# Kernel optimization log

Hardware: AMD Instinct MI355X
Metric: run time of the kernel (lower is better)

Reference implementation:

```python
import jax, jax.numpy as jnp
import numpy as np

N = 100000
E = 1600000
IN_C = 128
HID = 32
HEADS = 4
OUT_C = 16
G = 128
NEG_SLOPE = 0.2


def setup_inputs() -> dict:
    key = jax.random.key(0)
    ks = jax.random.split(key, 16)
    x = jax.random.normal(ks[0], (N, IN_C), dtype=jnp.float32)
    edge_index = jax.random.randint(ks[1], (2, E), 0, N, dtype=jnp.int64)
    batch = jnp.sort(jax.random.randint(ks[2], (N,), 0, G, dtype=jnp.int64))
    node_weights = jax.random.uniform(ks[3], (N, 1), dtype=jnp.float32)
    s = 1.0 / np.sqrt(IN_C)
    W1 = jax.random.uniform(ks[4], (IN_C, HEADS * HID), jnp.float32, -s, s)
    att_src1 = jax.random.uniform(ks[5], (HEADS, HID), jnp.float32, -s, s)
    att_dst1 = jax.random.uniform(ks[6], (HEADS, HID), jnp.float32, -s, s)
    b1 = jnp.zeros((HEADS * HID,), jnp.float32)
    s2 = 1.0 / np.sqrt(HEADS * HID)
    W2 = jax.random.uniform(ks[7], (HEADS * HID, HID), jnp.float32, -s2, s2)
    att_src2 = jax.random.uniform(ks[8], (1, HID), jnp.float32, -s2, s2)
    att_dst2 = jax.random.uniform(ks[9], (1, HID), jnp.float32, -s2, s2)
    b2 = jnp.zeros((HID,), jnp.float32)
    s3 = 1.0 / np.sqrt(HID)
    fcW = jax.random.uniform(ks[10], (HID, OUT_C), jnp.float32, -s3, s3)
    fcb = jax.random.uniform(ks[11], (OUT_C,), jnp.float32, -s3, s3)
    return {"x": x, "edge_index": edge_index, "batch": batch,
            "node_weights": node_weights,
            "W1": W1, "att_src1": att_src1, "att_dst1": att_dst1, "b1": b1,
            "W2": W2, "att_src2": att_src2, "att_dst2": att_dst2, "b2": b2,
            "fcW": fcW, "fcb": fcb}


def gat_conv(x, src, dst, W, att_src, att_dst, bias, heads, ch, concat):
    n = x.shape[0]
    h = (x @ W).reshape(n, heads, ch)                       # [N,H,C]
    a_src = jnp.sum(h * att_src[None], axis=-1)             # [N,H]
    a_dst = jnp.sum(h * att_dst[None], axis=-1)             # [N,H]
    e = jax.nn.leaky_relu(a_src[src] + a_dst[dst], NEG_SLOPE)  # [E,H]
    # segment softmax over incoming edges of each destination node
    e_max = jax.ops.segment_max(e, dst, num_segments=n)
    ex = jnp.exp(e - e_max[dst])
    denom = jax.ops.segment_sum(ex, dst, num_segments=n)
    alpha = ex / denom[dst]                                 # [E,H]
    msg = h[src] * alpha[..., None]                         # [E,H,C]
    out = jax.ops.segment_sum(msg, dst, num_segments=n)     # [N,H,C]
    if concat:
        out = out.reshape(n, heads * ch)
    else:
        out = out.mean(axis=1)
    return out + bias


def reference(x, edge_index, batch, node_weights,
              W1, att_src1, att_dst1, b1,
              W2, att_src2, att_dst2, b2,
              fcW, fcb):
    n = x.shape[0]
    # PyG GATConv adds self-loops by default
    loop = jnp.arange(n, dtype=edge_index.dtype)
    src = jnp.concatenate([edge_index[0], loop])
    dst = jnp.concatenate([edge_index[1], loop])

    h = x * node_weights
    h = jax.nn.elu(gat_conv(h, src, dst, W1, att_src1, att_dst1, b1, HEADS, HID, True))
    h = jax.nn.elu(gat_conv(h, src, dst, W2, att_src2, att_dst2, b2, 1, HID, False))
    # global mean pool over graphs
    sums = jax.ops.segment_sum(h, batch, num_segments=G)
    cnts = jax.ops.segment_sum(jnp.ones((n,), h.dtype), batch, num_segments=G)
    pooled = sums / jnp.maximum(cnts, 1.0)[:, None]
    return pooled @ fcW + fcb
```

## Files before the change

### kernel.cpp

```cpp
#include <hip/hip_runtime.h>
#include <cstdint>

#define OUT_C 16
#define NGRAPH 128
#define NEG 0.2f
#define NB_MAX 512
#define BSH 8
#define BSZ 256
#define CAP 8192

typedef unsigned int uint;
typedef unsigned short ushort;
typedef unsigned char uchar;
typedef __attribute__((ext_vector_type(8))) short bf16x8;
typedef __attribute__((ext_vector_type(4))) float f32x4;
typedef __attribute__((ext_vector_type(2))) float f32x2;

union U4B { uint4 u; bf16x8 v; };

__device__ __forceinline__ ushort f2bf(float f) {
  uint u = __float_as_uint(f);
  uint r = (u + 0x7FFF + ((u >> 16) & 1)) >> 16;
  return (ushort)r;
}

__device__ __forceinline__ int wave_incl_scan_i(int v) {
  int lane = threadIdx.x & 63;
#pragma unroll
  for (int off = 1; off < 64; off <<= 1) {
    int u = __shfl_up(v, off, 64);
    if (lane >= off) v += u;
  }
  return v;
}

__global__ void k_bin(const int* __restrict__ ei,
                      const float* __restrict__ W1, const float* __restrict__ W2,
                      ushort* __restrict__ Wt1, ushort* __restrict__ Wt2,
                      int E, int Etot, int NB, int nbin,
                      int* __restrict__ bcur, uint* __restrict__ bbuf) {
  if (blockIdx.x >= nbin) {
    int t2 = (blockIdx.x - nbin) * 256 + threadIdx.x;
    if (t2 < 16384) {
      int n = t2 >> 7, k = t2 & 127;
      Wt1[t2] = f2bf(W1[k * 128 + n]);
    } else {
      int u = t2 - 16384;
      int n = u >> 7, k = u & 127;
      Wt2[u] = f2bf(W2[k * 32 + n]);
    }
    return;
  }
  __shared__ int h[NB_MAX];
  __shared__ int baseo[NB_MAX];
  int t = threadIdx.x;
  for (int b = t; b < NB; b += 256) h[b] = 0;
  __syncthreads();
  int cbase = blockIdx.x * 4096;
  int cend = min(cbase + 4096, Etot);
  for (int e = cbase + t; e < cend; e += 256) {
    int d = (e < E) ? ei[E + e] : (e - E);
    atomicAdd(&h[d >> BSH], 1);
  }
  __syncthreads();
  for (int b = t; b < NB; b += 256) {
    int c = h[b];
    baseo[b] = c ? atomicAdd(&bcur[b], c) : 0;
    h[b] = 0;
  }
  __syncthreads();
  for (int e = cbase + t; e < cend; e += 256) {
    int s, d;
    if (e < E) { s = ei[e]; d = ei[E + e]; } else { s = e - E; d = s; }
    int b = d >> BSH;
    int r = atomicAdd(&h[b], 1);
    bbuf[(size_t)b * CAP + baseo[b] + r] = ((uint)(d & (BSZ - 1)) << 17) | (uint)s;
  }
}

__global__ void k_build(const uint* __restrict__ bbuf, const int* __restrict__ bcur,
                        int NB, int N, int* __restrict__ offs, int* __restrict__ ssrc) {
  __shared__ int sst[NB_MAX + 1];
  __shared__ int wsum2[4];
  __shared__ int deg[BSZ];
  int t = threadIdx.x, lane = t & 63, wid = t >> 6;
  int v0 = (2 * t < NB) ? bcur[2 * t] : 0;
  int v1 = (2 * t + 1 < NB) ? bcur[2 * t + 1] : 0;
  int s = v0 + v1;
  int sv = wave_incl_scan_i(s);
  if (lane == 63) wsum2[wid] = sv;
  deg[t] = 0;
  __syncthreads();
  if (t == 0) {
    int r = 0;
#pragma unroll
    for (int k = 0; k < 4; k++) { int x = wsum2[k]; wsum2[k] = r; r += x; }
  }
  __syncthreads();
  int excl = wsum2[wid] + sv - s;
  sst[2 * t] = excl;
  sst[2 * t + 1] = excl + v0;
  if (t == 255) sst[512] = excl + v0 + v1;
  __syncthreads();
  int b = blockIdx.x;
  int ebeg = sst[b], eend = sst[b + 1];
  int cnt = eend - ebeg;
  for (int i = t; i < cnt; i += BSZ)
    atomicAdd(&deg[bbuf[(size_t)b * CAP + i] >> 17], 1);
  __syncthreads();
  int v = deg[t];
  int sv2 = wave_incl_scan_i(v);
  if (lane == 63) wsum2[wid] = sv2;
  __syncthreads();
  if (t == 0) {
    int r = 0;
#pragma unroll
    for (int k = 0; k < 4; k++) { int x = wsum2[k]; wsum2[k] = r; r += x; }
  }
  __syncthreads();
  int excl2 = wsum2[wid] + sv2 - v;
  int node = (b << BSH) + t;
  if (node < N) offs[node] = ebeg + excl2;
  if (b == 0 && t == 0) offs[N] = sst[512];
  __syncthreads();
  deg[t] = excl2;
  __syncthreads();
  for (int i = t; i < cnt; i += BSZ) {
    uint rec = bbuf[(size_t)b * CAP + i];
    int r = atomicAdd(&deg[rec >> 17], 1);
    ssrc[ebeg + r] = (int)(rec & 0x1FFFF);
  }
}

__global__ void k_gemm1(const float* __restrict__ x, const ushort* __restrict__ Wt,
                        const float* __restrict__ nw, const float* __restrict__ att_s,
                        const float* __restrict__ att_d, uchar* __restrict__ hb1,
                        float* __restrict__ asrc, float* __restrict__ adst, int M) {
  int wv = threadIdx.x >> 6, l = threadIdx.x & 63;
  int lg = l >> 4, lr = l & 15;
  int row0 = blockIdx.x * 64 + wv * 16;
  int node = row0 + lr;
  bool valid = node < M;
  float sc = valid ? nw[node] : 0.f;
  bf16x8 afr[4];
  const float* xr = x + (size_t)node * 128;
#pragma unroll
  for (int kc = 0; kc < 4; kc++) {
    float v[8];
    if (valid) {
      float4 q0 = *reinterpret_cast<const float4*>(xr + kc * 32 + lg * 8);
      float4 q1 = *reinterpret_cast<const float4*>(xr + kc * 32 + lg * 8 + 4);
      v[0] = q0.x; v[1] = q0.y; v[2] = q0.z; v[3] = q0.w;
      v[4] = q1.x; v[5] = q1.y; v[6] = q1.z; v[7] = q1.w;
    } else {
#pragma unroll
      for (int j = 0; j < 8; j++) v[j] = 0.f;
    }
    U4B a;
    uint pk0 = (uint)f2bf(v[0] * sc) | ((uint)f2bf(v[1] * sc) << 16);
    uint pk1 = (uint)f2bf(v[2] * sc) | ((uint)f2bf(v[3] * sc) << 16);
    uint pk2 = (uint)f2bf(v[4] * sc) | ((uint)f2bf(v[5] * sc) << 16);
    uint pk3 = (uint)f2bf(v[6] * sc) | ((uint)f2bf(v[7] * sc) << 16);
    a.u = make_uint4(pk0, pk1, pk2, pk3);
    afr[kc] = a.v;
  }
  float pS[4][4], pD[4][4];
#pragma unroll
  for (int h = 0; h < 4; h++)
#pragma unroll
    for (int v = 0; v < 4; v++) { pS[h][v] = 0.f; pD[h][v] = 0.f; }
#pragma unroll
  for (int ct = 0; ct < 8; ct++) {
    f32x4 acc = {0.f, 0.f, 0.f, 0.f};
    const ushort* wrow = Wt + (size_t)(ct * 16 + lr) * 128;
#pragma unroll
    for (int kc = 0; kc < 4; kc++) {
      U4B bfr;
      bfr.u = *reinterpret_cast<const uint4*>(wrow + kc * 32 + lg * 8);
      acc = __builtin_amdgcn_mfma_f32_16x16x32_bf16(afr[kc], bfr.v, acc, 0, 0, 0);
    }
    int col = ct * 16 + lr;
    float asw = att_s[col], adw = att_d[col];
    int h = ct >> 1;
#pragma unroll
    for (int v = 0; v < 4; v++) {
      int nrow = row0 + lg * 4 + v;
      if (nrow < M) {
        uint b8 = (uint)__builtin_amdgcn_cvt_pk_fp8_f32(acc[v], acc[v], 0, false);
        hb1[(size_t)nrow * 128 + col] = (uchar)(b8 & 0xFF);
      }
      pS[h][v] += acc[v] * asw;
      pD[h][v] += acc[v] * adw;
    }
  }
#pragma unroll
  for (int off = 1; off < 16; off <<= 1) {
#pragma unroll
    for (int h = 0; h < 4; h++)
#pragma unroll
      for (int v = 0; v < 4; v++) {
        pS[h][v] += __shfl_xor(pS[h][v], off, 16);
        pD[h][v] += __shfl_xor(pD[h][v], off, 16);
      }
  }
  if (lr == 0) {
#pragma unroll
    for (int v = 0; v < 4; v++) {
      int n2 = row0 + lg * 4 + v;
      if (n2 < M) {
#pragma unroll
        for (int h = 0; h < 4; h++) {
          asrc[n2 * 4 + h] = pS[h][v];
          adst[n2 * 4 + h] = pD[h][v];
        }
      }
    }
  }
}

__global__ void k_gemm2(const ushort* __restrict__ A, const ushort* __restrict__ Wt,
                        const float* __restrict__ att_s, const float* __restrict__ att_d,
                        uchar* __restrict__ hb2, float* __restrict__ asrc,
                        float* __restrict__ adst, int M) {
  int wv = threadIdx.x >> 6, l = threadIdx.x & 63;
  int lg = l >> 4, lr = l & 15;
  int row0 = blockIdx.x * 64 + wv * 16;
  int node = row0 + lr;
  bool valid = node < M;
  bf16x8 afr[4];
#pragma unroll
  for (int kc = 0; kc < 4; kc++) {
    U4B a;
    if (valid) a.u = *reinterpret_cast<const uint4*>(A + (size_t)node * 128 + kc * 32 + lg * 8);
    else a.u = make_uint4(0, 0, 0, 0);
    afr[kc] = a.v;
  }
  float pS[4], pD[4];
#pragma unroll
  for (int v = 0; v < 4; v++) { pS[v] = 0.f; pD[v] = 0.f; }
#pragma unroll
  for (int ct = 0; ct < 2; ct++) {
    f32x4 acc = {0.f, 0.f, 0.f, 0.f};
    const ushort* wrow = Wt + (size_t)(ct * 16 + lr) * 128;
#pragma unroll
    for (int kc = 0; kc < 4; kc++) {
      U4B bfr;
      bfr.u = *reinterpret_cast<const uint4*>(wrow + kc * 32 + lg * 8);
      acc = __builtin_amdgcn_mfma_f32_16x16x32_bf16(afr[kc], bfr.v, acc, 0, 0, 0);
    }
    int col = ct * 16 + lr;
    float asw = att_s[col], adw = att_d[col];
#pragma unroll
    for (int v = 0; v < 4; v++) {
      int nrow = row0 + lg * 4 + v;
      if (nrow < M) {
        uint b8 = (uint)__builtin_amdgcn_cvt_pk_fp8_f32(acc[v], acc[v], 0, false);
        hb2[(size_t)nrow * 32 + col] = (uchar)(b8 & 0xFF);
      }
      pS[v] += acc[v] * asw;
      pD[v] += acc[v] * adw;
    }
  }
#pragma unroll
  for (int off = 1; off < 16; off <<= 1) {
#pragma unroll
    for (int v = 0; v < 4; v++) {
      pS[v] += __shfl_xor(pS[v], off, 16);
      pD[v] += __shfl_xor(pD[v], off, 16);
    }
  }
  if (lr == 0) {
#pragma unroll
    for (int v = 0; v < 4; v++) {
      int n2 = row0 + lg * 4 + v;
      if (n2 < M) { asrc[n2] = pS[v]; adst[n2] = pD[v]; }
    }
  }
}

__global__ void k_aggr1(const int* __restrict__ offs, const int* __restrict__ ssrc,
                        const uchar* __restrict__ hb, const float* __restrict__ asrc,
                        const float* __restrict__ adst, const float* __restrict__ bias,
                        ushort* __restrict__ outb, int N) {
  int wid = threadIdx.x >> 6, l = threadIdx.x & 63;
  int d = blockIdx.x * 4 + wid;
  if (d >= N) return;
  int slot = l >> 3;
  int k = l & 7;
  int h = k >> 1;
  float ad = adst[d * 4 + h];
  int beg = offs[d], end = offs[d + 1];
  float a[16] = {};
  float ds = 0.f;
  for (int i = beg; i < end; i += 8) {
    int e = i + slot;
    int ec = min(e, end - 1);
    int s = ssrc[ec];
    float xv = asrc[s * 4 + h] + ad;
    xv = xv > 0.f ? xv : NEG * xv;
    float w = __expf(xv);
    w = (e < end) ? w : 0.f;
    uint4 p = *reinterpret_cast<const uint4*>(hb + (size_t)s * 128 + k * 16);
    uint pu[4] = {p.x, p.y, p.z, p.w};
#pragma unroll
    for (int q = 0; q < 4; q++) {
      f32x2 f0 = __builtin_amdgcn_cvt_pk_f32_fp8(pu[q], false);
      f32x2 f1 = __builtin_amdgcn_cvt_pk_f32_fp8(pu[q], true);
      a[q * 4 + 0] += w * f0.x;
      a[q * 4 + 1] += w * f0.y;
      a[q * 4 + 2] += w * f1.x;
      a[q * 4 + 3] += w * f1.y;
    }
    ds += w;
  }
  int b3 = (l >> 3) & 1, b4 = (l >> 4) & 1, b5 = (l >> 5) & 1;
  float t8[8];
#pragma unroll
  for (int r = 0; r < 8; r++) {
    float send = b3 ? a[r] : a[r + 8];
    float recv = __shfl_xor(send, 8, 64);
    t8[r] = (b3 ? a[r + 8] : a[r]) + recv;
  }
  float t4[4];
#pragma unroll
  for (int r = 0; r < 4; r++) {
    float send = b4 ? t8[r] : t8[r + 4];
    float recv = __shfl_xor(send, 16, 64);
    t4[r] = (b4 ? t8[r + 4] : t8[r]) + recv;
  }
  float t2[2];
#pragma unroll
  for (int r = 0; r < 2; r++) {
    float send = b5 ? t4[r] : t4[r + 2];
    float recv = __shfl_xor(send, 32, 64);
    t2[r] = (b5 ? t4[r + 2] : t4[r]) + recv;
  }
  ds += __shfl_xor(ds, 8, 64);
  ds += __shfl_xor(ds, 16, 64);
  ds += __shfl_xor(ds, 32, 64);
  float inv = 1.f / ds;
  int c0 = k * 16 + b3 * 8 + b4 * 4 + b5 * 2;
  float r0 = t2[0] * inv + bias[c0];
  float r1 = t2[1] * inv + bias[c0 + 1];
  r0 = r0 > 0.f ? r0 : expm1f(r0);
  r1 = r1 > 0.f ? r1 : expm1f(r1);
  *reinterpret_cast<uint*>(outb + (size_t)d * 128 + c0) =
      (uint)f2bf(r0) | ((uint)f2bf(r1) << 16);
}

__global__ void k_aggr2(const int* __restrict__ offs, const int* __restrict__ ssrc,
                        const uchar* __restrict__ hb, const float* __restrict__ asrc,
                        const float* __restrict__ adst, const float* __restrict__ bias,
                        float* __restrict__ out, int N) {
  int wid = threadIdx.x >> 6, l = threadIdx.x & 63;
  int d = blockIdx.x * 4 + wid;
  if (d >= N) return;
  int slot = l >> 2;
  int k = l & 3;
  float ad = adst[d];
  int beg = offs[d], end = offs[d + 1];
  float a[8] = {};
  float ds = 0.f;
  for (int i = beg; i < end; i += 16) {
    int e = i + slot;
    int ec = min(e, end - 1);
    int s = ssrc[ec];
    float xv = asrc[s] + ad;
    xv = xv > 0.f ? xv : NEG * xv;
    float w = __expf(xv);
    w = (e < end) ? w : 0.f;
    uint2 p = *reinterpret_cast<const uint2*>(hb + (size_t)s * 32 + k * 8);
    f32x2 f0 = __builtin_amdgcn_cvt_pk_f32_fp8(p.x, false);
    f32x2 f1 = __builtin_amdgcn_cvt_pk_f32_fp8(p.x, true);
    f32x2 f2 = __builtin_amdgcn_cvt_pk_f32_fp8(p.y, false);
    f32x2 f3 = __builtin_amdgcn_cvt_pk_f32_fp8(p.y, true);
    a[0] += w * f0.x; a[1] += w * f0.y; a[2] += w * f1.x; a[3] += w * f1.y;
    a[4] += w * f2.x; a[5] += w * f2.y; a[6] += w * f3.x; a[7] += w * f3.y;
    ds += w;
  }
  int b2 = (l >> 2) & 1, b3 = (l >> 3) & 1, b4 = (l >> 4) & 1;
  float t4[4];
#pragma unroll
  for (int r = 0; r < 4; r++) {
    float send = b2 ? a[r] : a[r + 4];
    float recv = __shfl_xor(send, 4, 64);
    t4[r] = (b2 ? a[r + 4] : a[r]) + recv;
  }
  float t2[2];
#pragma unroll
  for (int r = 0; r < 2; r++) {
    float send = b3 ? t4[r] : t4[r + 2];
    float recv = __shfl_xor(send, 8, 64);
    t2[r] = (b3 ? t4[r + 2] : t4[r]) + recv;
  }
  float send = b4 ? t2[0] : t2[1];
  float recv = __shfl_xor(send, 16, 64);
  float t1 = (b4 ? t2[1] : t2[0]) + recv;
  t1 += __shfl_xor(t1, 32, 64);
  ds += __shfl_xor(ds, 4, 64);
  ds += __shfl_xor(ds, 8, 64);
  ds += __shfl_xor(ds, 16, 64);
  ds += __shfl_xor(ds, 32, 64);
  if (l < 32) {
    int c = k * 8 + b2 * 4 + b3 * 2 + b4;
    float r = t1 / ds + bias[c];
    r = r > 0.f ? r : expm1f(r);
    out[(size_t)d * 32 + c] = r;
  }
}

__global__ void k_pool_fc(const float* __restrict__ h2, const int* __restrict__ batch,
                          const float* __restrict__ fcW, const float* __restrict__ fcb,
                          float* __restrict__ out, int N) {
  int g = blockIdx.x;
  int lo = 0, hi = N;
  while (lo < hi) { int mid = (lo + hi) >> 1; if (batch[mid] < g) lo = mid + 1; else hi = mid; }
  int beg = lo;
  hi = N;
  while (lo < hi) { int mid = (lo + hi) >> 1; if (batch[mid] < g + 1) lo = mid + 1; else hi = mid; }
  int end = lo;
  int t = threadIdx.x, c = t & 31, sub = t >> 5;
  float acc = 0.f;
  for (int n = beg + sub; n < end; n += 8) acc += h2[(size_t)n * 32 + c];
  __shared__ float red[8][32];
  __shared__ float pooled[32];
  red[sub][c] = acc;
  __syncthreads();
  if (sub == 0) {
    float s = 0.f;
#pragma unroll
    for (int i = 0; i < 8; i++) s += red[i][c];
    float cnt = (float)(end - beg);
    pooled[c] = s / fmaxf(cnt, 1.f);
  }
  __syncthreads();
  if (t < 16) {
    float r = fcb[t];
#pragma unroll
    for (int cc = 0; cc < 32; cc++) r += pooled[cc] * fcW[cc * 16 + t];
    out[g * 16 + t] = r;
  }
}

extern "C" void kernel_launch(void* const* d_in, const int* in_sizes, int n_in,
                              void* d_out, int out_size, void* d_ws, size_t ws_size,
                              hipStream_t stream) {
  const float* x     = (const float*)d_in[0];
  const int*   ei    = (const int*)d_in[1];
  const int*   batch = (const int*)d_in[2];
  const float* nw    = (const float*)d_in[3];
  const float* W1    = (const float*)d_in[4];
  const float* as1w  = (const float*)d_in[5];
  const float* ad1w  = (const float*)d_in[6];
  const float* b1    = (const float*)d_in[7];
  const float* W2    = (const float*)d_in[8];
  const float* as2w  = (const float*)d_in[9];
  const float* ad2w  = (const float*)d_in[10];
  const float* b2    = (const float*)d_in[11];
  const float* fcW   = (const float*)d_in[12];
  const float* fcb   = (const float*)d_in[13];
  float* out = (float*)d_out;

  const int N = in_sizes[0] / 128;
  const int E = in_sizes[1] / 2;
  const int Etot = E + N;
  const int NB = (N + BSZ - 1) >> BSH;

  char* w = (char*)d_ws;
  size_t ofs = 0;
  auto alloc = [&](size_t bytes) {
    char* p = w + ofs;
    ofs += (bytes + 255) & ~(size_t)255;
    return p;
  };
  uchar*  hb1    = (uchar*)alloc((size_t)N * 128);
  ushort* out1b  = (ushort*)alloc((size_t)N * 128 * 2);
  uchar*  hb2    = (uchar*)alloc((size_t)N * 32);
  float*  h2     = (float*)alloc((size_t)N * 32 * 4);
  float*  asrc1  = (float*)alloc((size_t)N * 4 * 4);
  float*  adst1  = (float*)alloc((size_t)N * 4 * 4);
  float*  asrc2  = (float*)alloc((size_t)N * 4);
  float*  adst2  = (float*)alloc((size_t)N * 4);
  ushort* Wt1    = (ushort*)alloc(16384 * 2);
  ushort* Wt2    = (ushort*)alloc(4096 * 2);
  int*    bcur   = (int*)alloc((size_t)NB * 4);
  int*    offs   = (int*)alloc((size_t)(N + 1) * 4);
  uint*   bbuf   = (uint*)alloc((size_t)NB * CAP * 4);
  int*    ssrc   = (int*)alloc((size_t)Etot * 4);

  hipMemsetAsync(bcur, 0, (size_t)NB * 4, stream);

  const int nbin = (Etot + 4095) / 4096;
  k_bin<<<nbin + 80, 256, 0, stream>>>(ei, W1, W2, Wt1, Wt2, E, Etot, NB, nbin, bcur, bbuf);
  k_build<<<NB, BSZ, 0, stream>>>(bbuf, bcur, NB, N, offs, ssrc);

  k_gemm1<<<(N + 63) / 64, 256, 0, stream>>>(x, Wt1, nw, as1w, ad1w, hb1, asrc1, adst1, N);
  k_aggr1<<<(N + 3) / 4, 256, 0, stream>>>(offs, ssrc, hb1, asrc1, adst1, b1, out1b, N);

  k_gemm2<<<(N + 63) / 64, 256, 0, stream>>>(out1b, Wt2, as2w, ad2w, hb2, asrc2, adst2, N);
  k_aggr2<<<(N + 3) / 4, 256, 0, stream>>>(offs, ssrc, hb2, asrc2, adst2, b2, h2, N);

  k_pool_fc<<<NGRAPH, 256, 0, stream>>>(h2, batch, fcW, fcb, out, N);
}
```

Baseline: 325.9 us.

## Merge CSR build with first GEMM and transpose MFMA output for packed stores

Fuses the CSR build kernel and the first-layer GEMM into one launch, with block ranges split by blockIdx, so the two independent stages can run concurrently on the GPU. Both GEMMs swap the MFMA operand order so each lane holds four consecutive columns of one node. That lets the fp8 output be written as one packed 32-bit store instead of four byte stores, and shortens the attention-score reduction to cross-lane-group shuffles with vectorized stores. This adds register pressure and a larger fused kernel, and concurrency depends on block scheduling.

```diff
diff --git a/kernel.cpp b/kernel.cpp
--- a/kernel.cpp
+++ b/kernel.cpp
@@ -78,71 +78,73 @@
   }
 }
 
-__global__ void k_build(const uint* __restrict__ bbuf, const int* __restrict__ bcur,
-                        int NB, int N, int* __restrict__ offs, int* __restrict__ ssrc) {
+__global__ void k_bg(const uint* __restrict__ bbuf, const int* __restrict__ bcur,
+                     int NB, int N, int* __restrict__ offs, int* __restrict__ ssrc,
+                     const float* __restrict__ x, const ushort* __restrict__ Wt,
+                     const float* __restrict__ nw, const float* __restrict__ att_s,
+                     const float* __restrict__ att_d, uchar* __restrict__ hb1,
+                     float* __restrict__ asrc, float* __restrict__ adst) {
   __shared__ int sst[NB_MAX + 1];
   __shared__ int wsum2[4];
   __shared__ int deg[BSZ];
-  int t = threadIdx.x, lane = t & 63, wid = t >> 6;
-  int v0 = (2 * t < NB) ? bcur[2 * t] : 0;
-  int v1 = (2 * t + 1 < NB) ? bcur[2 * t + 1] : 0;
-  int s = v0 + v1;
-  int sv = wave_incl_scan_i(s);
-  if (lane == 63) wsum2[wid] = sv;
-  deg[t] = 0;
-  __syncthreads();
-  if (t == 0) {
-    int r = 0;
-#pragma unroll
-    for (int k = 0; k < 4; k++) { int x = wsum2[k]; wsum2[k] = r; r += x; }
-  }
-  __syncthreads();
-  int excl = wsum2[wid] + sv - s;
-  sst[2 * t] = excl;
-  sst[2 * t + 1] = excl + v0;
-  if (t == 255) sst[512] = excl + v0 + v1;
-  __syncthreads();
-  int b = blockIdx.x;
-  int ebeg = sst[b], eend = sst[b + 1];
-  int cnt = eend - ebeg;
-  for (int i = t; i < cnt; i += BSZ)
-    atomicAdd(&deg[bbuf[(size_t)b * CAP + i] >> 17], 1);
-  __syncthreads();
-  int v = deg[t];
-  int sv2 = wave_incl_scan_i(v);
-  if (lane == 63) wsum2[wid] = sv2;
-  __syncthreads();
-  if (t == 0) {
-    int r = 0;
-#pragma unroll
-    for (int k = 0; k < 4; k++) { int x = wsum2[k]; wsum2[k] = r; r += x; }
-  }
-  __syncthreads();
-  int excl2 = wsum2[wid] + sv2 - v;
-  int node = (b << BSH) + t;
-  if (node < N) offs[node] = ebeg + excl2;
-  if (b == 0 && t == 0) offs[N] = sst[512];
-  __syncthreads();
-  deg[t] = excl2;
-  __syncthreads();
-  for (int i = t; i < cnt; i += BSZ) {
-    uint rec = bbuf[(size_t)b * CAP + i];
-    int r = atomicAdd(&deg[rec >> 17], 1);
-    ssrc[ebeg + r] = (int)(rec & 0x1FFFF);
-  }
-}
-
-__global__ void k_gemm1(const float* __restrict__ x, const ushort* __restrict__ Wt,
-                        const float* __restrict__ nw, const float* __restrict__ att_s,
-                        const float* __restrict__ att_d, uchar* __restrict__ hb1,
-                        float* __restrict__ asrc, float* __restrict__ adst, int M) {
+  if (blockIdx.x < (uint)NB) {
+    int t = threadIdx.x, lane = t & 63, wid = t >> 6;
+    int v0 = (2 * t < NB) ? bcur[2 * t] : 0;
+    int v1 = (2 * t + 1 < NB) ? bcur[2 * t + 1] : 0;
+    int s = v0 + v1;
+    int sv = wave_incl_scan_i(s);
+    if (lane == 63) wsum2[wid] = sv;
+    deg[t] = 0;
+    __syncthreads();
+    if (t == 0) {
+      int r = 0;
+#pragma unroll
+      for (int k = 0; k < 4; k++) { int x2 = wsum2[k]; wsum2[k] = r; r += x2; }
+    }
+    __syncthreads();
+    int excl = wsum2[wid] + sv - s;
+    sst[2 * t] = excl;
+    sst[2 * t + 1] = excl + v0;
+    if (t == 255) sst[512] = excl + v0 + v1;
+    __syncthreads();
+    int b = blockIdx.x;
+    int ebeg = sst[b], eend = sst[b + 1];
+    int cnt = eend - ebeg;
+    for (int i = t; i < cnt; i += BSZ)
+      atomicAdd(&deg[bbuf[(size_t)b * CAP + i] >> 17], 1);
+    __syncthreads();
+    int v = deg[t];
+    int sv2 = wave_incl_scan_i(v);
+    if (lane == 63) wsum2[wid] = sv2;
+    __syncthreads();
+    if (t == 0) {
+      int r = 0;
+#pragma unroll
+      for (int k = 0; k < 4; k++) { int x2 = wsum2[k]; wsum2[k] = r; r += x2; }
+    }
+    __syncthreads();
+    int excl2 = wsum2[wid] + sv2 - v;
+    int node = (b << BSH) + t;
+    if (node < N) offs[node] = ebeg + excl2;
+    if (b == 0 && t == 0) offs[N] = sst[512];
+    __syncthreads();
+    deg[t] = excl2;
+    __syncthreads();
+    for (int i = t; i < cnt; i += BSZ) {
+      uint rec = bbuf[(size_t)b * CAP + i];
+      int r = atomicAdd(&deg[rec >> 17], 1);
+      ssrc[ebeg + r] = (int)(rec & 0x1FFFF);
+    }
+    return;
+  }
+  int bid = blockIdx.x - NB;
   int wv = threadIdx.x >> 6, l = threadIdx.x & 63;
   int lg = l >> 4, lr = l & 15;
-  int row0 = blockIdx.x * 64 + wv * 16;
+  int row0 = bid * 64 + wv * 16;
   int node = row0 + lr;
-  bool valid = node < M;
+  bool valid = node < N;
   float sc = valid ? nw[node] : 0.f;
-  bf16x8 afr[4];
+  bf16x8 xfr[4];
   const float* xr = x + (size_t)node * 128;
 #pragma unroll
   for (int kc = 0; kc < 4; kc++) {
@@ -162,13 +164,9 @@
     uint pk2 = (uint)f2bf(v[4] * sc) | ((uint)f2bf(v[5] * sc) << 16);
     uint pk3 = (uint)f2bf(v[6] * sc) | ((uint)f2bf(v[7] * sc) << 16);
     a.u = make_uint4(pk0, pk1, pk2, pk3);
-    afr[kc] = a.v;
-  }
-  float pS[4][4], pD[4][4];
-#pragma unroll
-  for (int h = 0; h < 4; h++)
-#pragma unroll
-    for (int v = 0; v < 4; v++) { pS[h][v] = 0.f; pD[h][v] = 0.f; }
+    xfr[kc] = a.v;
+  }
+  float pS[4] = {}, pD[4] = {};
 #pragma unroll
   for (int ct = 0; ct < 8; ct++) {
     f32x4 acc = {0.f, 0.f, 0.f, 0.f};
@@ -177,44 +175,31 @@
     for (int kc = 0; kc < 4; kc++) {
       U4B bfr;
       bfr.u = *reinterpret_cast<const uint4*>(wrow + kc * 32 + lg * 8);
-      acc = __builtin_amdgcn_mfma_f32_16x16x32_bf16(afr[kc], bfr.v, acc, 0, 0, 0);
-    }
-    int col = ct * 16 + lr;
-    float asw = att_s[col], adw = att_d[col];
+      acc = __builtin_amdgcn_mfma_f32_16x16x32_bf16(bfr.v, xfr[kc], acc, 0, 0, 0);
+    }
+    int c0 = ct * 16 + lg * 4;
+    if (valid) {
+      uint u8 = (uint)__builtin_amdgcn_cvt_pk_fp8_f32(acc[0], acc[1], 0, false);
+      u8 = (uint)__builtin_amdgcn_cvt_pk_fp8_f32(acc[2], acc[3], u8, true);
+      *reinterpret_cast<uint*>(hb1 + (size_t)node * 128 + c0) = u8;
+    }
+    float4 as4 = *reinterpret_cast<const float4*>(att_s + c0);
+    float4 ad4 = *reinterpret_cast<const float4*>(att_d + c0);
     int h = ct >> 1;
-#pragma unroll
-    for (int v = 0; v < 4; v++) {
-      int nrow = row0 + lg * 4 + v;
-      if (nrow < M) {
-        uint b8 = (uint)__builtin_amdgcn_cvt_pk_fp8_f32(acc[v], acc[v], 0, false);
-        hb1[(size_t)nrow * 128 + col] = (uchar)(b8 & 0xFF);
-      }
-      pS[h][v] += acc[v] * asw;
-      pD[h][v] += acc[v] * adw;
-    }
-  }
-#pragma unroll
-  for (int off = 1; off < 16; off <<= 1) {
-#pragma unroll
-    for (int h = 0; h < 4; h++)
-#pragma unroll
-      for (int v = 0; v < 4; v++) {
-        pS[h][v] += __shfl_xor(pS[h][v], off, 16);
-        pD[h][v] += __shfl_xor(pD[h][v], off, 16);
-      }
-  }
-  if (lr == 0) {
-#pragma unroll
-    for (int v = 0; v < 4; v++) {
-      int n2 = row0 + lg * 4 + v;
-      if (n2 < M) {
-#pragma unroll
-        for (int h = 0; h < 4; h++) {
-          asrc[n2 * 4 + h] = pS[h][v];
-          adst[n2 * 4 + h] = pD[h][v];
-        }
-      }
-    }
+    pS[h] += acc[0] * as4.x + acc[1] * as4.y + acc[2] * as4.z + acc[3] * as4.w;
+    pD[h] += acc[0] * ad4.x + acc[1] * ad4.y + acc[2] * ad4.z + acc[3] * ad4.w;
+  }
+#pragma unroll
+  for (int off = 16; off < 64; off <<= 1) {
+#pragma unroll
+    for (int h = 0; h < 4; h++) {
+      pS[h] += __shfl_xor(pS[h], off, 64);
+      pD[h] += __shfl_xor(pD[h], off, 64);
+    }
+  }
+  if (lg == 0 && valid) {
+    *reinterpret_cast<float4*>(asrc + node * 4) = make_float4(pS[0], pS[1], pS[2], pS[3]);
+    *reinterpret_cast<float4*>(adst + node * 4) = make_float4(pD[0], pD[1], pD[2], pD[3]);
   }
 }
 
@@ -235,9 +220,7 @@
     else a.u = make_uint4(0, 0, 0, 0);
     afr[kc] = a.v;
   }
-  float pS[4], pD[4];
-#pragma unroll
-  for (int v = 0; v < 4; v++) { pS[v] = 0.f; pD[v] = 0.f; }
+  float pS = 0.f, pD = 0.f;
 #pragma unroll
   for (int ct = 0; ct < 2; ct++) {
     f32x4 acc = {0.f, 0.f, 0.f, 0.f};
@@ -246,36 +229,25 @@
     for (int kc = 0; kc < 4; kc++) {
       U4B bfr;
       bfr.u = *reinterpret_cast<const uint4*>(wrow + kc * 32 + lg * 8);
-      acc = __builtin_amdgcn_mfma_f32_16x16x32_bf16(afr[kc], bfr.v, acc, 0, 0, 0);
-    }
-    int col = ct * 16 + lr;
-    float asw = att_s[col], adw = att_d[col];
-#pragma unroll
-    for (int v = 0; v < 4; v++) {
-      int nrow = row0 + lg * 4 + v;
-      if (nrow < M) {
-        uint b8 = (uint)__builtin_amdgcn_cvt_pk_fp8_f32(acc[v], acc[v], 0, false);
-        hb2[(size_t)nrow * 32 + col] = (uchar)(b8 & 0xFF);
-      }
-      pS[v] += acc[v] * asw;
-      pD[v] += acc[v] * adw;
-    }
-  }
-#pragma unroll
-  for (int off = 1; off < 16; off <<= 1) {
-#pragma unroll
-    for (int v = 0; v < 4; v++) {
-      pS[v] += __shfl_xor(pS[v], off, 16);
-      pD[v] += __shfl_xor(pD[v], off, 16);
-    }
-  }
-  if (lr == 0) {
-#pragma unroll
-    for (int v = 0; v < 4; v++) {
-      int n2 = row0 + lg * 4 + v;
-      if (n2 < M) { asrc[n2] = pS[v]; adst[n2] = pD[v]; }
-    }
-  }
+      acc = __builtin_amdgcn_mfma_f32_16x16x32_bf16(bfr.v, afr[kc], acc, 0, 0, 0);
+    }
+    int c0 = ct * 16 + lg * 4;
+    if (valid) {
+      uint u8 = (uint)__builtin_amdgcn_cvt_pk_fp8_f32(acc[0], acc[1], 0, false);
+      u8 = (uint)__builtin_amdgcn_cvt_pk_fp8_f32(acc[2], acc[3], u8, true);
+      *reinterpret_cast<uint*>(hb2 + (size_t)node * 32 + c0) = u8;
+    }
+    float4 as4 = *reinterpret_cast<const float4*>(att_s + c0);
+    float4 ad4 = *reinterpret_cast<const float4*>(att_d + c0);
+    pS += acc[0] * as4.x + acc[1] * as4.y + acc[2] * as4.z + acc[3] * as4.w;
+    pD += acc[0] * ad4.x + acc[1] * ad4.y + acc[2] * ad4.z + acc[3] * ad4.w;
+  }
+#pragma unroll
+  for (int off = 16; off < 64; off <<= 1) {
+    pS += __shfl_xor(pS, off, 64);
+    pD += __shfl_xor(pD, off, 64);
+  }
+  if (lg == 0 && valid) { asrc[node] = pS; adst[node] = pD; }
 }
 
 __global__ void k_aggr1(const int* __restrict__ offs, const int* __restrict__ ssrc,
@@ -492,9 +464,11 @@
 
   const int nbin = (Etot + 4095) / 4096;
   k_bin<<<nbin + 80, 256, 0, stream>>>(ei, W1, W2, Wt1, Wt2, E, Etot, NB, nbin, bcur, bbuf);
-  k_build<<<NB, BSZ, 0, stream>>>(bbuf, bcur, NB, N, offs, ssrc);
-
-  k_gemm1<<<(N + 63) / 64, 256, 0, stream>>>(x, Wt1, nw, as1w, ad1w, hb1, asrc1, adst1, N);
+
+  const int ngemm1 = (N + 63) / 64;
+  k_bg<<<NB + ngemm1, 256, 0, stream>>>(bbuf, bcur, NB, N, offs, ssrc,
+                                        x, Wt1, nw, as1w, ad1w, hb1, asrc1, adst1);
+
   k_aggr1<<<(N + 3) / 4, 256, 0, stream>>>(offs, ssrc, hb1, asrc1, adst1, b1, out1b, N);
 
   k_gemm2<<<(N + 63) / 64, 256, 0, stream>>>(out1b, Wt2, as2w, ad2w, hb2, asrc2, adst2, N);
```

Result: faster. 314.3 us (-3.6%).
